# Performance work log

Measured on AMD Instinct MI355X. Metric: run time of the kernel, lower is better.

## Reference

```python
import jax, jax.numpy as jnp
import numpy as np

D_IN = 1024
D_OUT = 1024
SEQ = 4096


def setup_inputs() -> dict:
    key = jax.random.key(0)
    kx, kq, kk, kv = jax.random.split(key, 4)
    x = jax.random.normal(kx, (SEQ, D_IN), dtype=jnp.float32)
    # torch.rand -> uniform [0,1)
    wquery = jax.random.uniform(kq, (D_IN, D_OUT), dtype=jnp.float32)
    wkey = jax.random.uniform(kk, (D_IN, D_OUT), dtype=jnp.float32)
    wvalue = jax.random.uniform(kv, (D_IN, D_OUT), dtype=jnp.float32)
    return {"x": x, "wquery": wquery, "wkey": wkey, "wvalue": wvalue}


def reference(x, wquery, wkey, wvalue):
    keys = x @ wkey          # [S, d_out]
    queries = x @ wquery     # [S, d_out]
    values = x @ wvalue      # [S, d_out]
    scale = 1.0 / jnp.sqrt(jnp.float32(keys.shape[-1]))
    attn_scores = queries @ keys.T            # [S, S]
    attn_weights = jax.nn.softmax(attn_scores * scale, axis=-1)
    context = attn_weights @ values           # [S, d_out]
    return context
```

## Files before the change

kernel.cpp:

```cpp
#include <hip/hip_runtime.h>
#include <math.h>

#define SEQ 4096
#define DIM 1024

typedef _Float16 f16;
typedef _Float16 f16x8 __attribute__((ext_vector_type(8)));
typedef _Float16 f16x4 __attribute__((ext_vector_type(4)));
typedef float f32x4 __attribute__((ext_vector_type(4)));

#define GLOAD_LDS16(g, l)                                              \
    __builtin_amdgcn_global_load_lds(                                  \
        (const __attribute__((address_space(1))) void*)(g),            \
        (__attribute__((address_space(3))) void*)(l), 16, 0, 0)

__global__ __launch_bounds__(256) void split16rs(const float* __restrict__ in,
                                                 f16* __restrict__ hi,
                                                 f16* __restrict__ lo,
                                                 float* __restrict__ sx) {
    __shared__ float sred[4];
    const int tid = threadIdx.x;
    const int i = blockIdx.x * 256 + tid;
    const float4 v = ((const float4*)in)[i];
    const float vv[4] = {v.x, v.y, v.z, v.w};
    f16x4 h, l;
#pragma unroll
    for (int q = 0; q < 4; ++q) {
        const f16 hq = (f16)vv[q];
        h[q] = hq;
        l[q] = (f16)(vv[q] - (float)hq);
    }
    ((f16x4*)hi)[i] = h;
    ((f16x4*)lo)[i] = l;
    float s = v.x + v.y + v.z + v.w;
#pragma unroll
    for (int m = 32; m >= 1; m >>= 1) s += __shfl_xor(s, m);
    if ((tid & 63) == 0) sred[tid >> 6] = s;
    __syncthreads();
    if (tid == 0) sx[blockIdx.x] = sred[0] + sred[1] + sred[2] + sred[3];
}

__global__ __launch_bounds__(256) void wtrans3h(
    const float* __restrict__ Wq, const float* __restrict__ Wk,
    const float* __restrict__ Wv,
    f16* __restrict__ QT, f16* __restrict__ KT, f16* __restrict__ VT) {
    __shared__ float tile[32][33];
    const int tid = threadIdx.x;
    const int r0 = blockIdx.x * 32;
    const int c0 = blockIdx.y * 32;
    const int z = blockIdx.z;
    const float* W = (z == 0) ? Wq : (z == 1) ? Wk : Wv;
    f16* T = (z == 0) ? QT : (z == 1) ? KT : VT;
    const float off = (z < 2) ? 0.5f : 0.0f;
    {
        const int r = tid >> 3, c = (tid & 7) * 4;
        const float4 v = *(const float4*)&W[(size_t)(r0 + r) * DIM + c0 + c];
        tile[r][c + 0] = v.x;
        tile[r][c + 1] = v.y;
        tile[r][c + 2] = v.z;
        tile[r][c + 3] = v.w;
    }
    __syncthreads();
    {
        const int n = tid >> 3;
        const int k = (tid & 7) * 4;
        f16x4 h;
#pragma unroll
        for (int q = 0; q < 4; ++q) h[q] = (f16)(tile[k + q][n] - off);
        *(f16x4*)&T[(size_t)(c0 + n) * DIM + r0 + k] = h;
    }
}

__global__ __launch_bounds__(256) void rowsum_hl(
    const f16* __restrict__ Qh, const f16* __restrict__ Ql,
    const f16* __restrict__ Kh, const f16* __restrict__ Kl,
    float* __restrict__ rq, float* __restrict__ rk) {
    const f16 *H, *L;
    float* out;
    if (blockIdx.y == 0) { H = Qh; L = Ql; out = rq; }
    else                 { H = Kh; L = Kl; out = rk; }
    const int row = blockIdx.x * 4 + (threadIdx.x >> 6);
    const int lane = threadIdx.x & 63;
    const f16x8* h8 = (const f16x8*)(H + (size_t)row * DIM);
    const f16x8* l8 = (const f16x8*)(L + (size_t)row * DIM);
    float s = 0.f;
#pragma unroll
    for (int c = 0; c < 2; ++c) {
        const f16x8 a = h8[lane + 64 * c];
        const f16x8 b = l8[lane + 64 * c];
#pragma unroll
        for (int e = 0; e < 8; ++e) s += (float)a[e] + (float)b[e];
    }
#pragma unroll
    for (int m = 32; m >= 1; m >>= 1) s += __shfl_xor(s, m);
    if (lane == 0) out[row] = s;
}

#define EPI_F32 0
#define EPI_SPLIT16 1
#define EPI_TRANS16 2

template <int NPAIR, int KTILES>
__global__ __launch_bounds__(256, 2) void gemm128s(
    const f16* __restrict__ A0, const f16* __restrict__ A1, int ldA, int ldB,
    const f16* __restrict__ B0_0, const f16* __restrict__ B1_0,
    void* o0_0, void* o1_0,
    const f16* __restrict__ B0_1, const f16* __restrict__ B1_1,
    void* o0_1, void* o1_1,
    const f16* __restrict__ B0_2, const f16* __restrict__ B1_2,
    void* o0_2, void* o1_2,
    int aoffPerSet, int boffPerSet,
    int epi0, int epi1, int epi2,
    int N, float scale) {
    __shared__ __align__(16) f16 As[2][128 * 64];
    __shared__ __align__(16) f16 Bs[2][128 * 64];

    const int tid = threadIdx.x;
    const int lane = tid & 63;
    const int wid = tid >> 6;
    const int wr = wid >> 1, wc = wid & 1;

    const int total = (int)(gridDim.y << 5);
    int lid = (int)blockIdx.y * 32 + (int)blockIdx.x;
    lid = (lid & 7) * (total >> 3) + (lid >> 3);
    const int bx = lid & 31;
    int by = lid >> 5;

    const int set = by >> 3;
    by &= 7;

    const f16 *B0, *B1;
    void *o0, *o1;
    int epi;
    if (set == 0)      { B0 = B0_0; B1 = B1_0; o0 = o0_0; o1 = o1_0; epi = epi0; }
    else if (set == 1) { B0 = B0_1; B1 = B1_1; o0 = o0_1; o1 = o1_1; epi = epi1; }
    else               { B0 = B0_2; B1 = B1_2; o0 = o0_2; o1 = o1_2; epi = epi2; }
    const int aoff = set * aoffPerSet;
    const int boff = set * boffPerSet;

    const int m0 = bx * 128;
    const int n0 = by * 128;

    const f16* APs[2] = {A0, A1};
    const f16* BPs[2] = {B0, B1};
    const int nt = NPAIR * KTILES;

    f32x4 acc[4][4];
#pragma unroll
    for (int i = 0; i < 4; ++i)
#pragma unroll
        for (int j = 0; j < 4; ++j) acc[i][j] = (f32x4){0.f, 0.f, 0.f, 0.f};

    auto STAGE = [&](int t, int b) {
        const int pass = t / KTILES;
        const int k0 = (t % KTILES) * 64;
        const f16* Ap = APs[pass];
        const f16* Bp = BPs[pass];
#pragma unroll
        for (int L = 0; L < 4; ++L) {
            const int idx = L * 256 + tid;
            const int row = idx >> 3;
            const int sc = ((idx & 7) * 16) ^ ((row & 7) << 4);
            const int ldsu = (L * 256 + (tid & ~63)) * 8;
            GLOAD_LDS16(Ap + (size_t)(m0 + row) * ldA + k0 + (sc >> 1) + aoff,
                        &As[b][ldsu]);
            GLOAD_LDS16(Bp + (size_t)(n0 + row) * ldB + k0 + (sc >> 1) + boff,
                        &Bs[b][ldsu]);
        }
    };

    STAGE(0, 0);

    for (int t = 0; t < nt; ++t) {
        const int cur = t & 1;
        __builtin_amdgcn_s_barrier();
        asm volatile("" ::: "memory");
        if (t + 1 < nt) {
            STAGE(t + 1, cur ^ 1);
            asm volatile("s_waitcnt vmcnt(8)" ::: "memory");
        } else {
            asm volatile("s_waitcnt vmcnt(0)" ::: "memory");
        }
        __builtin_amdgcn_s_barrier();
        asm volatile("" ::: "memory");

#pragma unroll
        for (int kk = 0; kk < 2; ++kk) {
            const int cb = kk * 64 + (lane >> 4) * 16;
            f16x8 af[4], bv[4];
#pragma unroll
            for (int i = 0; i < 4; ++i) {
                const int r = wr * 64 + i * 16 + (lane & 15);
                af[i] = *(const f16x8*)(&As[cur][r * 64 +
                                                 ((cb ^ ((r & 7) << 4)) >> 1)]);
            }
#pragma unroll
            for (int j = 0; j < 4; ++j) {
                const int r = wc * 64 + j * 16 + (lane & 15);
                bv[j] = *(const f16x8*)(&Bs[cur][r * 64 +
                                                 ((cb ^ ((r & 7) << 4)) >> 1)]);
            }
            __builtin_amdgcn_s_setprio(1);
#pragma unroll
            for (int i = 0; i < 4; ++i)
#pragma unroll
                for (int j = 0; j < 4; ++j)
                    acc[i][j] = __builtin_amdgcn_mfma_f32_16x16x32_f16(
                        af[i], bv[j], acc[i][j], 0, 0, 0);
            __builtin_amdgcn_s_setprio(0);
        }
    }

    const int row0 = m0 + wr * 64 + (lane >> 4) * 4;
    const int col0 = n0 + wc * 64 + (lane & 15);

    if (epi == EPI_F32) {
        float* O = (float*)o0;
#pragma unroll
        for (int i = 0; i < 4; ++i)
#pragma unroll
            for (int j = 0; j < 4; ++j)
#pragma unroll
                for (int q = 0; q < 4; ++q)
                    O[(size_t)(row0 + i * 16 + q) * N + col0 + j * 16] =
                        acc[i][j][q] * scale;
    } else if (epi == EPI_SPLIT16) {
        f16* Hi = (f16*)o0;
        f16* Lo = (f16*)o1;
#pragma unroll
        for (int i = 0; i < 4; ++i)
#pragma unroll
            for (int j = 0; j < 4; ++j)
#pragma unroll
                for (int q = 0; q < 4; ++q) {
                    const float x = acc[i][j][q];
                    const f16 h = (f16)x;
                    const size_t idx = (size_t)(row0 + i * 16 + q) * N + col0 + j * 16;
                    Hi[idx] = h;
                    Lo[idx] = (f16)(x - (float)h);
                }
    } else {
        f16* OT = (f16*)o0;
#pragma unroll
        for (int i = 0; i < 4; ++i)
#pragma unroll
            for (int j = 0; j < 4; ++j) {
                f16x4 v;
#pragma unroll
                for (int q = 0; q < 4; ++q) v[q] = (f16)acc[i][j][q];
                *(f16x4*)&OT[(size_t)(col0 + j * 16) * SEQ + row0 + i * 16] = v;
            }
    }
}

template <int NPAIR, int KT>
__global__ __launch_bounds__(512, 2) void qkrank1(
    const f16* __restrict__ A0, const f16* __restrict__ B0,
    const f16* __restrict__ A1, const f16* __restrict__ B1,
    const float* __restrict__ sx, const float* __restrict__ rq,
    const float* __restrict__ rk,
    f16* __restrict__ Pu, float* __restrict__ Mp, float* __restrict__ Lp) {
    constexpr int K = KT * 64;
    constexpr int nt = NPAIR * KT;
    __shared__ __align__(16) f16 As[2][256 * 64];
    __shared__ __align__(16) f16 Bs[2][256 * 64];

    const int tid = threadIdx.x;
    const int lane = tid & 63;
    const int wid = tid >> 6;
    const int wr = wid >> 2;
    const int wc = wid & 3;

    const int wg = ((int)blockIdx.x & 7) * 32 + ((int)blockIdx.x >> 3);
    const int m0 = (wg >> 4) * 256;
    const int n0 = (wg & 15) * 256;
    const int bcol = n0 >> 8;

    const f16* APs[2] = {A0, A1};
    const f16* BPs[2] = {B0, B1};

    f32x4 acc[8][4];
#pragma unroll
    for (int i = 0; i < 8; ++i)
#pragma unroll
        for (int j = 0; j < 4; ++j) acc[i][j] = (f32x4){0.f, 0.f, 0.f, 0.f};

    auto STAGE = [&](int t, int b) {
        const f16* Ap = APs[t / KT];
        const f16* Bp = BPs[t / KT];
        const int k0 = (t % KT) * 64;
#pragma unroll
        for (int L = 0; L < 4; ++L) {
            const int idx = L * 512 + tid;
            const int row = idx >> 3;
            const int sc = ((idx & 7) * 16) ^ ((row & 7) << 4);
            const int ldsu = (L * 512 + (tid & ~63)) * 8;
            GLOAD_LDS16(Ap + (size_t)(m0 + row) * K + k0 + (sc >> 1),
                        &As[b][ldsu]);
            GLOAD_LDS16(Bp + (size_t)(n0 + row) * K + k0 + (sc >> 1),
                        &Bs[b][ldsu]);
        }
    };

    STAGE(0, 0);

    for (int t = 0; t < nt; ++t) {
        const int cur = t & 1;
        __builtin_amdgcn_s_barrier();
        asm volatile("" ::: "memory");
        if (t + 1 < nt) {
            STAGE(t + 1, cur ^ 1);
            asm volatile("s_waitcnt vmcnt(8)" ::: "memory");
        } else {
            asm volatile("s_waitcnt vmcnt(0)" ::: "memory");
        }
        __builtin_amdgcn_s_barrier();
        asm volatile("" ::: "memory");

#pragma unroll
        for (int kk = 0; kk < 2; ++kk) {
            const int cb = kk * 64 + (lane >> 4) * 16;
            f16x8 af[8], bv[4];
#pragma unroll
            for (int i = 0; i < 8; ++i) {
                const int r = wr * 128 + i * 16 + (lane & 15);
                af[i] = *(const f16x8*)(&As[cur][r * 64 +
                                                 ((cb ^ ((r & 7) << 4)) >> 1)]);
            }
#pragma unroll
            for (int j = 0; j < 4; ++j) {
                const int r = wc * 64 + j * 16 + (lane & 15);
                bv[j] = *(const f16x8*)(&Bs[cur][r * 64 +
                                                 ((cb ^ ((r & 7) << 4)) >> 1)]);
            }
            __builtin_amdgcn_s_setprio(1);
#pragma unroll
            for (int i = 0; i < 8; ++i)
#pragma unroll
                for (int j = 0; j < 4; ++j)
                    acc[i][j] = __builtin_amdgcn_mfma_f32_16x16x32_f16(
                        af[i], bv[j], acc[i][j], 0, 0, 0);
            __builtin_amdgcn_s_setprio(0);
        }
    }

    const int g4 = lane >> 4;
    const int l15 = lane & 15;
    const int row0 = m0 + wr * 128 + g4 * 4;
    const int col0 = n0 + wc * 64 + l15;
    float u[4], w4[4];
#pragma unroll
    for (int j = 0; j < 4; ++j) {
        const float sxc = sx[col0 + j * 16];
        u[j] = 256.f * sxc + 0.5f * rk[col0 + j * 16];
        w4[j] = 0.5f * sxc;
    }
#pragma unroll
    for (int i = 0; i < 8; ++i)
#pragma unroll
        for (int q = 0; q < 4; ++q) {
            const int r = row0 + i * 16 + q;
            const float sxr = sx[r];
            const float rqr = rq[r];
#pragma unroll
            for (int j = 0; j < 4; ++j)
                acc[i][j][q] =
                    (acc[i][j][q] + sxr * u[j] + rqr * w4[j]) * 0.03125f;
        }

    float* partm = (float*)&As[0][0];
    float* mrow  = partm + 1024;
    float* parts = mrow + 256;
    float red[8][4];
#pragma unroll
    for (int i = 0; i < 8; ++i)
#pragma unroll
        for (int q = 0; q < 4; ++q) {
            float v = acc[i][0][q];
#pragma unroll
            for (int j = 1; j < 4; ++j) v = fmaxf(v, acc[i][j][q]);
            red[i][q] = v;
        }
#pragma unroll
    for (int msk = 1; msk < 16; msk <<= 1)
#pragma unroll
        for (int i = 0; i < 8; ++i)
#pragma unroll
            for (int q = 0; q < 4; ++q)
                red[i][q] = fmaxf(red[i][q], __shfl_xor(red[i][q], msk));
    __syncthreads();
    if (l15 == 0)
#pragma unroll
        for (int i = 0; i < 8; ++i)
#pragma unroll
            for (int q = 0; q < 4; ++q)
                partm[(wr * 128 + i * 16 + g4 * 4 + q) * 4 + wc] = red[i][q];
    __syncthreads();
    if (tid < 256) {
        const float* p = partm + tid * 4;
        mrow[tid] = fmaxf(fmaxf(p[0], p[1]), fmaxf(p[2], p[3]));
    }
    __syncthreads();
#pragma unroll
    for (int i = 0; i < 8; ++i)
#pragma unroll
        for (int q = 0; q < 4; ++q) {
            const float mB = mrow[wr * 128 + i * 16 + g4 * 4 + q];
            float s = 0.f;
#pragma unroll
            for (int j = 0; j < 4; ++j) {
                const float e = __expf(acc[i][j][q] - mB);
                acc[i][j][q] = e;
                s += e;
            }
            red[i][q] = s;
        }
#pragma unroll
    for (int msk = 1; msk < 16; msk <<= 1)
#pragma unroll
        for (int i = 0; i < 8; ++i)
#pragma unroll
            for (int q = 0; q < 4; ++q) red[i][q] += __shfl_xor(red[i][q], msk);
    if (l15 == 0)
#pragma unroll
        for (int i = 0; i < 8; ++i)
#pragma unroll
            for (int q = 0; q < 4; ++q)
                parts[(wr * 128 + i * 16 + g4 * 4 + q) * 4 + wc] = red[i][q];
    __syncthreads();
    if (tid < 256) {
        const float* p = parts + tid * 4;
        Mp[(size_t)(m0 + tid) * 16 + bcol] = mrow[tid];
        Lp[(size_t)(m0 + tid) * 16 + bcol] = p[0] + p[1] + p[2] + p[3];
    }
#pragma unroll
    for (int i = 0; i < 8; ++i)
#pragma unroll
        for (int q = 0; q < 4; ++q) {
            const size_t r = row0 + i * 16 + q;
#pragma unroll
            for (int j = 0; j < 4; ++j)
                Pu[r * SEQ + col0 + j * 16] = (f16)acc[i][j][q];
        }
}

__global__ __launch_bounds__(256) void rowfix(const float* __restrict__ Mp,
                                              const float* __restrict__ Lp,
                                              f16* __restrict__ Pu) {
    __shared__ float mls[32];
    const int tid = threadIdx.x;
    const size_t r = blockIdx.x;
    if (tid < 32)
        mls[tid] = (tid < 16) ? Mp[r * 16 + tid] : Lp[r * 16 + tid - 16];
    __syncthreads();
    float m = -1e30f;
#pragma unroll
    for (int b = 0; b < 16; ++b) m = fmaxf(m, mls[b]);
    float l = 0.f;
#pragma unroll
    for (int b = 0; b < 16; ++b) l += __expf(mls[b] - m) * mls[16 + b];
    const float inv = 1.f / l;

    f16* row = Pu + r * SEQ;
#pragma unroll
    for (int p = 0; p < 2; ++p) {
        const int c0 = p * 2048 + tid * 8;
        const float d = __expf(mls[c0 >> 8] - m) * inv;
        f16x8 v = *(const f16x8*)(row + c0);
#pragma unroll
        for (int e = 0; e < 8; ++e) v[e] = (f16)((float)v[e] * d);
        *(f16x8*)(row + c0) = v;
    }
}

__global__ __launch_bounds__(256) void addf(const float* __restrict__ a,
                                            const float* __restrict__ b,
                                            float* __restrict__ o) {
    const int i = blockIdx.x * 256 + threadIdx.x;
    const float4 x = ((const float4*)a)[i];
    const float4 y = ((const float4*)b)[i];
    ((float4*)o)[i] = make_float4(x.x + y.x, x.y + y.y, x.z + y.z, x.w + y.w);
}

extern "C" void kernel_launch(void* const* d_in, const int* in_sizes, int n_in,
                              void* d_out, int out_size, void* d_ws, size_t ws_size,
                              hipStream_t stream) {
    const float* x  = (const float*)d_in[0];
    const float* wq = (const float*)d_in[1];
    const float* wk = (const float*)d_in[2];
    const float* wv = (const float*)d_in[3];
    float* O = (float*)d_out;

    char* ws = (char*)d_ws;
    const size_t MB = 1024 * 1024;
    const size_t KB = 1024;
    f16* Qh = (f16*)(ws + 0 * MB);
    f16* Ql = (f16*)(ws + 8 * MB);
    f16* Kh = (f16*)(ws + 16 * MB);
    f16* VT = (f16*)(ws + 24 * MB);
    float* sx = (float*)(ws + 32 * MB);
    float* rq = (float*)(ws + 32 * MB + 16 * KB);
    float* rk = (float*)(ws + 32 * MB + 32 * KB);
    float* Mp = (float*)(ws + 32 * MB + 48 * KB);
    float* Lp = (float*)(ws + 32 * MB + 304 * KB);
    f16* Pu = (f16*)(ws + 40 * MB);
    float* P0 = (float*)(ws + 72 * MB);
    float* P1 = (float*)(ws + 88 * MB);
    f16* Xh  = (f16*)(ws + 40 * MB);
    f16* Xl  = (f16*)(ws + 48 * MB);
    f16* Wqh = (f16*)(ws + 56 * MB);
    f16* Wkh = (f16*)(ws + 58 * MB);
    f16* Wvh = (f16*)(ws + 60 * MB);
    f16* Kl  = (f16*)(ws + 64 * MB);

    split16rs<<<4096, 256, 0, stream>>>(x, Xh, Xl, sx);
    wtrans3h<<<dim3(DIM / 32, DIM / 32, 3), 256, 0, stream>>>(
        wq, wk, wv, Wqh, Wkh, Wvh);

    gemm128s<2, 16><<<dim3(32, 24), 256, 0, stream>>>(
        Xh, Xl, DIM, DIM,
        Wqh, Wqh, Qh, Ql,
        Wkh, Wkh, Kh, Kl,
        Wvh, Wvh, VT, nullptr,
        0, 0,
        EPI_SPLIT16, EPI_SPLIT16, EPI_TRANS16,
        DIM, 1.f);

    rowsum_hl<<<dim3(1024, 2), 256, 0, stream>>>(Qh, Ql, Kh, Kl, rq, rk);

    qkrank1<2, 16><<<256, 512, 0, stream>>>(
        Qh, Kh, Ql, Kh, sx, rq, rk, Pu, Mp, Lp);

    rowfix<<<4096, 256, 0, stream>>>(Mp, Lp, Pu);

    gemm128s<1, 32><<<dim3(32, 16), 256, 0, stream>>>(
        Pu, Pu, SEQ, SEQ,
        VT, VT, P0, nullptr,
        VT, VT, P1, nullptr,
        VT, VT, P1, nullptr,
        2048, 2048,
        EPI_F32, EPI_F32, EPI_F32,
        DIM, 1.f);

    addf<<<4096, 256, 0, stream>>>(P0, P1, O);
}
```

Baseline: 227.7 us.

## Fuse softmax rescale into PV GEMM and row sums into projection epilogue

Removes the rowfix pass, which rewrote the whole 4096x4096 fp16 probability matrix, by computing per-strip scale factors in a tiny mkD kernel and applying them in a new pvstrip GEMM, accumulating per 256-column strip. The rowsum_hl kernel is also removed: the projection GEMM epilogue computes Q and K row sums with shuffles plus atomicAdd, which also makes the K low-half buffer unnecessary. This costs a second accumulator set (more registers), extra per-strip FMA work in the GEMM, atomic contention, and a memset. Row sums now come from fp32 accumulators instead of hi+lo halves, and summation order becomes nondeterministic.

```diff
diff --git a/kernel.cpp b/kernel.cpp
--- a/kernel.cpp
+++ b/kernel.cpp
@@ -71,31 +71,6 @@
     }
 }
 
-__global__ __launch_bounds__(256) void rowsum_hl(
-    const f16* __restrict__ Qh, const f16* __restrict__ Ql,
-    const f16* __restrict__ Kh, const f16* __restrict__ Kl,
-    float* __restrict__ rq, float* __restrict__ rk) {
-    const f16 *H, *L;
-    float* out;
-    if (blockIdx.y == 0) { H = Qh; L = Ql; out = rq; }
-    else                 { H = Kh; L = Kl; out = rk; }
-    const int row = blockIdx.x * 4 + (threadIdx.x >> 6);
-    const int lane = threadIdx.x & 63;
-    const f16x8* h8 = (const f16x8*)(H + (size_t)row * DIM);
-    const f16x8* l8 = (const f16x8*)(L + (size_t)row * DIM);
-    float s = 0.f;
-#pragma unroll
-    for (int c = 0; c < 2; ++c) {
-        const f16x8 a = h8[lane + 64 * c];
-        const f16x8 b = l8[lane + 64 * c];
-#pragma unroll
-        for (int e = 0; e < 8; ++e) s += (float)a[e] + (float)b[e];
-    }
-#pragma unroll
-    for (int m = 32; m >= 1; m >>= 1) s += __shfl_xor(s, m);
-    if (lane == 0) out[row] = s;
-}
-
 #define EPI_F32 0
 #define EPI_SPLIT16 1
 #define EPI_TRANS16 2
@@ -109,7 +84,7 @@
     void* o0_1, void* o1_1,
     const f16* __restrict__ B0_2, const f16* __restrict__ B1_2,
     void* o0_2, void* o1_2,
-    int aoffPerSet, int boffPerSet,
+    float* rs0, float* rs1,
     int epi0, int epi1, int epi2,
     int N, float scale) {
     __shared__ __align__(16) f16 As[2][128 * 64];
@@ -132,11 +107,10 @@
     const f16 *B0, *B1;
     void *o0, *o1;
     int epi;
-    if (set == 0)      { B0 = B0_0; B1 = B1_0; o0 = o0_0; o1 = o1_0; epi = epi0; }
-    else if (set == 1) { B0 = B0_1; B1 = B1_1; o0 = o0_1; o1 = o1_1; epi = epi1; }
-    else               { B0 = B0_2; B1 = B1_2; o0 = o0_2; o1 = o1_2; epi = epi2; }
-    const int aoff = set * aoffPerSet;
-    const int boff = set * boffPerSet;
+    float* rs;
+    if (set == 0)      { B0 = B0_0; B1 = B1_0; o0 = o0_0; o1 = o1_0; epi = epi0; rs = rs0; }
+    else if (set == 1) { B0 = B0_1; B1 = B1_1; o0 = o0_1; o1 = o1_1; epi = epi1; rs = rs1; }
+    else               { B0 = B0_2; B1 = B1_2; o0 = o0_2; o1 = o1_2; epi = epi2; rs = nullptr; }
 
     const int m0 = bx * 128;
     const int n0 = by * 128;
@@ -162,9 +136,9 @@
             const int row = idx >> 3;
             const int sc = ((idx & 7) * 16) ^ ((row & 7) << 4);
             const int ldsu = (L * 256 + (tid & ~63)) * 8;
-            GLOAD_LDS16(Ap + (size_t)(m0 + row) * ldA + k0 + (sc >> 1) + aoff,
+            GLOAD_LDS16(Ap + (size_t)(m0 + row) * ldA + k0 + (sc >> 1),
                         &As[b][ldsu]);
-            GLOAD_LDS16(Bp + (size_t)(n0 + row) * ldB + k0 + (sc >> 1) + boff,
+            GLOAD_LDS16(Bp + (size_t)(n0 + row) * ldB + k0 + (sc >> 1),
                         &Bs[b][ldsu]);
         }
     };
@@ -237,8 +211,22 @@
                     const f16 h = (f16)x;
                     const size_t idx = (size_t)(row0 + i * 16 + q) * N + col0 + j * 16;
                     Hi[idx] = h;
-                    Lo[idx] = (f16)(x - (float)h);
+                    if (Lo) Lo[idx] = (f16)(x - (float)h);
                 }
+        if (rs) {
+#pragma unroll
+            for (int i = 0; i < 4; ++i)
+#pragma unroll
+                for (int q = 0; q < 4; ++q) {
+                    float rsum = acc[i][0][q] + acc[i][1][q] +
+                                 acc[i][2][q] + acc[i][3][q];
+#pragma unroll
+                    for (int msk = 1; msk < 16; msk <<= 1)
+                        rsum += __shfl_xor(rsum, msk);
+                    if ((lane & 15) == 0)
+                        atomicAdd(&rs[row0 + i * 16 + q], rsum);
+                }
+        }
     } else {
         f16* OT = (f16*)o0;
 #pragma unroll
@@ -444,33 +432,144 @@
         }
 }
 
-__global__ __launch_bounds__(256) void rowfix(const float* __restrict__ Mp,
-                                              const float* __restrict__ Lp,
-                                              f16* __restrict__ Pu) {
-    __shared__ float mls[32];
+__global__ __launch_bounds__(256) void mkD(const float* __restrict__ Mp,
+                                           const float* __restrict__ Lp,
+                                           float* __restrict__ D) {
+    const size_t r = blockIdx.x * 256 + threadIdx.x;
+    float mv[16], lv[16];
+#pragma unroll
+    for (int b = 0; b < 16; ++b) mv[b] = Mp[r * 16 + b];
+#pragma unroll
+    for (int b = 0; b < 16; ++b) lv[b] = Lp[r * 16 + b];
+    float m = mv[0];
+#pragma unroll
+    for (int b = 1; b < 16; ++b) m = fmaxf(m, mv[b]);
+    float l = 0.f;
+#pragma unroll
+    for (int b = 0; b < 16; ++b) l += __expf(mv[b] - m) * lv[b];
+    const float inv = 1.f / l;
+#pragma unroll
+    for (int b = 0; b < 16; ++b) D[r * 16 + b] = __expf(mv[b] - m) * inv;
+}
+
+template <int KTILES>
+__global__ __launch_bounds__(256, 2) void pvstrip(
+    const f16* __restrict__ Pu, const f16* __restrict__ VT,
+    const float* __restrict__ D,
+    float* __restrict__ P0, float* __restrict__ P1) {
+    __shared__ __align__(16) f16 As[2][128 * 64];
+    __shared__ __align__(16) f16 Bs[2][128 * 64];
+
     const int tid = threadIdx.x;
-    const size_t r = blockIdx.x;
-    if (tid < 32)
-        mls[tid] = (tid < 16) ? Mp[r * 16 + tid] : Lp[r * 16 + tid - 16];
-    __syncthreads();
-    float m = -1e30f;
-#pragma unroll
-    for (int b = 0; b < 16; ++b) m = fmaxf(m, mls[b]);
-    float l = 0.f;
-#pragma unroll
-    for (int b = 0; b < 16; ++b) l += __expf(mls[b] - m) * mls[16 + b];
-    const float inv = 1.f / l;
-
-    f16* row = Pu + r * SEQ;
-#pragma unroll
-    for (int p = 0; p < 2; ++p) {
-        const int c0 = p * 2048 + tid * 8;
-        const float d = __expf(mls[c0 >> 8] - m) * inv;
-        f16x8 v = *(const f16x8*)(row + c0);
-#pragma unroll
-        for (int e = 0; e < 8; ++e) v[e] = (f16)((float)v[e] * d);
-        *(f16x8*)(row + c0) = v;
-    }
+    const int lane = tid & 63;
+    const int wid = tid >> 6;
+    const int wr = wid >> 1, wc = wid & 1;
+
+    const int total = (int)(gridDim.y << 5);
+    int lid = (int)blockIdx.y * 32 + (int)blockIdx.x;
+    lid = (lid & 7) * (total >> 3) + (lid >> 3);
+    const int bx = lid & 31;
+    int by = lid >> 5;
+    const int set = by >> 3;
+    by &= 7;
+    float* Out = set ? P1 : P0;
+    const int koff = set * 2048;
+    const int strip0 = set * 8;
+
+    const int m0 = bx * 128;
+    const int n0 = by * 128;
+    const int row0 = m0 + wr * 64 + (lane >> 4) * 4;
+    const int col0 = n0 + wc * 64 + (lane & 15);
+
+    f32x4 acc[4][4], acc2[4][4];
+#pragma unroll
+    for (int i = 0; i < 4; ++i)
+#pragma unroll
+        for (int j = 0; j < 4; ++j) {
+            acc[i][j] = (f32x4){0.f, 0.f, 0.f, 0.f};
+            acc2[i][j] = (f32x4){0.f, 0.f, 0.f, 0.f};
+        }
+
+    auto STAGE = [&](int t, int b) {
+        const int k0 = t * 64 + koff;
+#pragma unroll
+        for (int L = 0; L < 4; ++L) {
+            const int idx = L * 256 + tid;
+            const int row = idx >> 3;
+            const int sc = ((idx & 7) * 16) ^ ((row & 7) << 4);
+            const int ldsu = (L * 256 + (tid & ~63)) * 8;
+            GLOAD_LDS16(Pu + (size_t)(m0 + row) * SEQ + k0 + (sc >> 1),
+                        &As[b][ldsu]);
+            GLOAD_LDS16(VT + (size_t)(n0 + row) * SEQ + k0 + (sc >> 1),
+                        &Bs[b][ldsu]);
+        }
+    };
+
+    STAGE(0, 0);
+
+    for (int t = 0; t < KTILES; ++t) {
+        const int cur = t & 1;
+        __builtin_amdgcn_s_barrier();
+        asm volatile("" ::: "memory");
+        if (t + 1 < KTILES) {
+            STAGE(t + 1, cur ^ 1);
+            asm volatile("s_waitcnt vmcnt(8)" ::: "memory");
+        } else {
+            asm volatile("s_waitcnt vmcnt(0)" ::: "memory");
+        }
+        __builtin_amdgcn_s_barrier();
+        asm volatile("" ::: "memory");
+
+#pragma unroll
+        for (int kk = 0; kk < 2; ++kk) {
+            const int cb = kk * 64 + (lane >> 4) * 16;
+            f16x8 af[4], bv[4];
+#pragma unroll
+            for (int i = 0; i < 4; ++i) {
+                const int r = wr * 64 + i * 16 + (lane & 15);
+                af[i] = *(const f16x8*)(&As[cur][r * 64 +
+                                                 ((cb ^ ((r & 7) << 4)) >> 1)]);
+            }
+#pragma unroll
+            for (int j = 0; j < 4; ++j) {
+                const int r = wc * 64 + j * 16 + (lane & 15);
+                bv[j] = *(const f16x8*)(&Bs[cur][r * 64 +
+                                                 ((cb ^ ((r & 7) << 4)) >> 1)]);
+            }
+            __builtin_amdgcn_s_setprio(1);
+#pragma unroll
+            for (int i = 0; i < 4; ++i)
+#pragma unroll
+                for (int j = 0; j < 4; ++j)
+                    acc[i][j] = __builtin_amdgcn_mfma_f32_16x16x32_f16(
+                        af[i], bv[j], acc[i][j], 0, 0, 0);
+            __builtin_amdgcn_s_setprio(0);
+        }
+
+        if ((t & 3) == 3) {
+            const int strip = strip0 + (t >> 2);
+#pragma unroll
+            for (int i = 0; i < 4; ++i)
+#pragma unroll
+                for (int q = 0; q < 4; ++q) {
+                    const float dv = D[(size_t)(row0 + i * 16 + q) * 16 + strip];
+#pragma unroll
+                    for (int j = 0; j < 4; ++j) {
+                        acc2[i][j][q] += dv * acc[i][j][q];
+                        acc[i][j][q] = 0.f;
+                    }
+                }
+        }
+    }
+
+#pragma unroll
+    for (int i = 0; i < 4; ++i)
+#pragma unroll
+        for (int j = 0; j < 4; ++j)
+#pragma unroll
+            for (int q = 0; q < 4; ++q)
+                Out[(size_t)(row0 + i * 16 + q) * DIM + col0 + j * 16] =
+                    acc2[i][j][q];
 }
 
 __global__ __launch_bounds__(256) void addf(const float* __restrict__ a,
@@ -503,6 +602,7 @@
     float* rk = (float*)(ws + 32 * MB + 32 * KB);
     float* Mp = (float*)(ws + 32 * MB + 48 * KB);
     float* Lp = (float*)(ws + 32 * MB + 304 * KB);
+    float* D  = (float*)(ws + 33 * MB);
     f16* Pu = (f16*)(ws + 40 * MB);
     float* P0 = (float*)(ws + 72 * MB);
     float* P1 = (float*)(ws + 88 * MB);
@@ -511,36 +611,28 @@
     f16* Wqh = (f16*)(ws + 56 * MB);
     f16* Wkh = (f16*)(ws + 58 * MB);
     f16* Wvh = (f16*)(ws + 60 * MB);
-    f16* Kl  = (f16*)(ws + 64 * MB);
 
     split16rs<<<4096, 256, 0, stream>>>(x, Xh, Xl, sx);
     wtrans3h<<<dim3(DIM / 32, DIM / 32, 3), 256, 0, stream>>>(
         wq, wk, wv, Wqh, Wkh, Wvh);
 
+    hipMemsetAsync(rq, 0, 32 * KB, stream);
+
     gemm128s<2, 16><<<dim3(32, 24), 256, 0, stream>>>(
         Xh, Xl, DIM, DIM,
         Wqh, Wqh, Qh, Ql,
-        Wkh, Wkh, Kh, Kl,
+        Wkh, Wkh, Kh, nullptr,
         Wvh, Wvh, VT, nullptr,
-        0, 0,
+        rq, rk,
         EPI_SPLIT16, EPI_SPLIT16, EPI_TRANS16,
         DIM, 1.f);
 
-    rowsum_hl<<<dim3(1024, 2), 256, 0, stream>>>(Qh, Ql, Kh, Kl, rq, rk);
-
     qkrank1<2, 16><<<256, 512, 0, stream>>>(
         Qh, Kh, Ql, Kh, sx, rq, rk, Pu, Mp, Lp);
 
-    rowfix<<<4096, 256, 0, stream>>>(Mp, Lp, Pu);
-
-    gemm128s<1, 32><<<dim3(32, 16), 256, 0, stream>>>(
-        Pu, Pu, SEQ, SEQ,
-        VT, VT, P0, nullptr,
-        VT, VT, P1, nullptr,
-        VT, VT, P1, nullptr,
-        2048, 2048,
-        EPI_F32, EPI_F32, EPI_F32,
-        DIM, 1.f);
+    mkD<<<16, 256, 0, stream>>>(Mp, Lp, D);
+
+    pvstrip<32><<<dim3(32, 16), 256, 0, stream>>>(Pu, VT, D, P0, P1);
 
     addf<<<4096, 256, 0, stream>>>(P0, P1, O);
 }
```

Result: no change. 224.9 us (median of 2 runs) (-1.2%).
